# Kernel optimization log

Measured on AMD Instinct MI355X. Metric: run time of the kernel, lower is better.

The kernel has to match this reference:

```python
import jax, jax.numpy as jnp
import numpy as np

B, C, L, HEADS, DK = 32, 128, 32, 8, 64  # batch, channels, lattice side (L1=L2=L), heads, head dim
NLAYER = 4


def setup_inputs() -> dict:
    key = jax.random.key(0)
    ks = jax.random.split(key, 6)
    s_in = 1.0 / float(np.sqrt(C))          # lecun-normal scale for QKV (fan_in = channels)
    s_out = 1.0 / float(np.sqrt(HEADS * DK))  # lecun-normal scale for W0 (fan_in = dk*heads)
    return {
        "x": jax.random.normal(ks[0], (B, C, L, L), jnp.float32),
        "Wq": jax.random.normal(ks[1], (HEADS * DK, C), jnp.float32) * s_in,
        "Wk": jax.random.normal(ks[2], (HEADS * DK, C), jnp.float32) * s_in,
        "Wv": jax.random.normal(ks[3], (HEADS * DK, C), jnp.float32) * s_in,
        "R": jax.random.normal(ks[4], (HEADS, L, L), jnp.float32) * 0.02,
        "W0": jax.random.normal(ks[5], (C, HEADS * DK), jnp.float32) * s_out,
    }


def get_irpe(R):
    # r[h, i, j] = R[h, (xi - xj) mod L1, (yi - yj) mod L2]  (jnp negative indexing wraps)
    heads, L1, L2 = R.shape
    a1 = jnp.arange(L1)
    a2 = jnp.arange(L2)
    dx = (a1[:, None] - a1[None, :]) % L1        # (L1, L1)
    dy = (a2[:, None] - a2[None, :]) % L2        # (L2, L2)
    bias = R[:, dx[:, None, :, None], dy[None, :, None, :]]  # (heads, L1, L2, L1, L2)
    return bias.reshape(heads, L1 * L2, L1 * L2)


def reference(x, Wq, Wk, Wv, R, W0):
    bias = get_irpe(R)                            # (heads, N, N)
    inv_layer = 1.0 / float(np.sqrt(NLAYER + 1))
    inv_sqrt_dk = 1.0 / float(np.sqrt(DK))

    def block(xs):  # xs: (C, L, L) — single sample, as in the original __call__
        xn = xs * inv_layer
        xf = xn.reshape(C, -1)                    # (C, N)
        Q = (Wq @ xf).reshape(HEADS, DK, -1)      # 1x1 conv == matmul
        K = (Wk @ xf).reshape(HEADS, DK, -1)
        V = (Wv @ xf).reshape(HEADS, DK, -1)
        dot = jnp.einsum('hdi,hdj->hij', Q, K) + bias
        alpha = jax.nn.softmax(dot * inv_sqrt_dk, axis=-1)
        att = jnp.einsum('hij,hdj->hdi', alpha, V).reshape(HEADS * DK, -1)
        return (W0 @ att).reshape(xs.shape) + xs  # residual

    return jax.vmap(block)(x)
```

## Files before the change

kernel.cpp:

```cpp
#include <hip/hip_runtime.h>


#define NB   32
#define NH   8
#define SEQ  1024
#define DKH  64
#define HDIM 512
#define CIN  128

#define SCL 0.18033688011112042f

typedef __bf16 bf16x8 __attribute__((ext_vector_type(8)));
typedef float floatx4 __attribute__((ext_vector_type(4)));
typedef unsigned short u16x8 __attribute__((ext_vector_type(8)));
typedef unsigned int uintx4 __attribute__((ext_vector_type(4)));

__device__ __forceinline__ unsigned short f2bf(float f) {
    union { float f; unsigned int u; } c; c.f = f;
    unsigned int u = c.u;
    return (unsigned short)((u + 0x7fffu + ((u >> 16) & 1u)) >> 16);
}
__device__ __forceinline__ bf16x8 ldfrag(const unsigned short* p) {
    u16x8 v = *reinterpret_cast<const u16x8*>(p);
    return __builtin_bit_cast(bf16x8, v);
}
__device__ __forceinline__ unsigned int pkbf(float a, float b) {
    unsigned int ua = __builtin_bit_cast(unsigned int, a);
    unsigned int ub = __builtin_bit_cast(unsigned int, b);
    ua += 0x7fffu + ((ua >> 16) & 1u);
    ub += 0x7fffu + ((ub >> 16) & 1u);
    return __builtin_amdgcn_perm(ub, ua, 0x07060302u);
}
__device__ __forceinline__ unsigned int pkbf_t(float a, float b) {
    return __builtin_amdgcn_perm(__builtin_bit_cast(unsigned int, b),
                                 __builtin_bit_cast(unsigned int, a), 0x07060302u);
}
__device__ __forceinline__ void g2l16(const void* g, void* l) {
    __builtin_amdgcn_global_load_lds((const __attribute__((address_space(1))) void*)g,
                                     (__attribute__((address_space(3))) void*)l, 16, 0, 0);
}


__global__ __launch_bounds__(256) void prep_all(const float* __restrict__ Wq,
                                                const float* __restrict__ Wk,
                                                const float* __restrict__ Wv,
                                                const float* __restrict__ W0,
                                                const float* __restrict__ R,
                                                const float* __restrict__ x,
                                                unsigned short* __restrict__ w2,
                                                unsigned short* __restrict__ w0f,
                                                float* __restrict__ biasG,
                                                unsigned short* __restrict__ xt2) {
    __shared__ float lds[64 * 65];
    int bid = blockIdx.x;
    if (bid < 256) {
        int gidx = bid * 256 + threadIdx.x;
        int lane = gidx & 63, slot = gidx >> 6;
        int bb = slot & 1, a = (slot >> 1) & 1, dxx = (slot >> 2) & 31, h = slot >> 7;
        int q = lane >> 4, n = lane & 15;
        int iy = (a << 4) + n;
        const float* Rh = R + (h << 10) + (dxx << 5);
        floatx4 v;
        for (int r = 0; r < 4; ++r) {
            int jy = (bb << 4) + 4 * q + r;
            v[r] = Rh[(iy - jy) & 31] * SCL;
        }
        *(floatx4*)&biasG[(size_t)gidx * 4] = v;
    } else if (bid < 1280) {
        int idx = (bid - 256) * 256 + threadIdx.x;
        if (idx < 196608) {
            int row = idx >> 7, col = idx & 127;
            float v;
            if (row < 512)       v = Wq[idx] * SCL;
            else if (row < 1024) v = Wk[idx - 65536];
            else                 v = Wv[idx - 131072];
            int rt = row >> 4, nr = row & 15, kc = col >> 5, qc = (col & 31) >> 3, jc = col & 7;
            w2[((rt * 4 + kc) * 512) + (qc * 16 + nr) * 8 + jc] = f2bf(v);
        } else {
            int idx2 = idx - 196608;
            int row = idx2 >> 9, col = idx2 & 511;
            int rt = row >> 4, nr = row & 15, kcA = col >> 5, qc = (col & 31) >> 3, jc = col & 7;
            w0f[((rt * 16 + kcA) * 512) + (qc * 16 + nr) * 8 + jc] = f2bf(W0[idx2]);
        }
    } else {
        int r = bid - 1280;
        int b = r & 31, yy = (r >> 5) & 1, zz = r >> 6;
        int c0 = yy * 64, p0 = zz * 64;
        int t = threadIdx.x, tr = t >> 6, tc = t & 63;
        const float inv_layer = 0.44721359549995793f;
        for (int rr = 0; rr < 16; ++rr) {
            int cl = rr * 4 + tr;
            lds[cl * 65 + tc] = x[(b * CIN + c0 + cl) * SEQ + p0 + tc];
        }
        __syncthreads();
        for (int rr = 0; rr < 16; ++rr) {
            int pl = rr * 4 + tr;
            int pos = p0 + pl, c = c0 + tc;
            int pt = pos >> 4, np = pos & 15, kc = c >> 5, qc = (c & 31) >> 3, jc = c & 7;
            xt2[((size_t)((b * 64 + pt) * 4 + kc) * 512) + (qc * 16 + np) * 8 + jc] =
                f2bf(lds[tc * 65 + pl] * inv_layer);
        }
    }
}

__global__ __launch_bounds__(256, 4) void qkv_gemm(const unsigned short* __restrict__ xt2,
                                                   const unsigned short* __restrict__ w2,
                                                   unsigned short* __restrict__ Qt,
                                                   unsigned short* __restrict__ Kf,
                                                   unsigned short* __restrict__ Vf) {
    int b = blockIdx.x, y = blockIdx.y, zt = blockIdx.z;
    int tid = threadIdx.x, wave = tid >> 6, lane = tid & 63, q = lane >> 4, n = lane & 15;
    floatx4 acc[4];
    for (int s = 0; s < 4; ++s) acc[s] = (floatx4){0.f, 0.f, 0.f, 0.f};
    bf16x8 af[4], bfr[4][4];
    if (y < 16) {
        int rt = y * 4 + wave;
        const unsigned short* wbase = w2 + (size_t)rt * 4 * 512 + lane * 8;
        const unsigned short* xbase = xt2 + (size_t)(b * 64 + zt * 4) * 4 * 512 + lane * 8;
        for (int kc = 0; kc < 4; ++kc) af[kc] = ldfrag(wbase + kc * 512);
        for (int s = 0; s < 4; ++s)
            for (int kc = 0; kc < 4; ++kc) bfr[s][kc] = ldfrag(xbase + (s * 4 + kc) * 512);
        for (int kc = 0; kc < 4; ++kc)
            for (int s = 0; s < 4; ++s)
                acc[s] = __builtin_amdgcn_mfma_f32_16x16x32_bf16(af[kc], bfr[s][kc], acc[s], 0, 0, 0);
        int wrow0 = y * 64 + wave * 16;
        int pos0 = zt * 64;
        if (y < 8) {
            int h = wrow0 >> 6;
            int d0 = (wrow0 & 63) + 4 * q;
            for (int s = 0; s < 4; ++s) {
                uint2 pk;
                pk.x = pkbf(acc[s][0], acc[s][1]);
                pk.y = pkbf(acc[s][2], acc[s][3]);
                int pos = pos0 + 16 * s + n;
                *(uint2*)&Qt[((size_t)(b * NH + h) * SEQ + pos) * DKH + d0] = pk;
            }
        } else {
            int h = (wrow0 >> 6) - 8;
            int bh = b * NH + h;
            int cd = wave >> 1;
            int qk = 2 * (wave & 1) + (q >> 1);
            int jk = 4 * (q & 1);
            for (int s = 0; s < 4; ++s) {
                uint2 pk;
                pk.x = pkbf(acc[s][0], acc[s][1]);
                pk.y = pkbf(acc[s][2], acc[s][3]);
                size_t addr = ((size_t)(bh * 16 + zt) * 8 + s * 2 + cd) * 512
                              + (qk * 16 + n) * 8 + jk;
                *(uint2*)&Kf[addr] = pk;
            }
        }
    } else {
        int pt = zt * 4 + wave;
        const unsigned short* xbase = xt2 + (size_t)((b * 64 + pt) * 4) * 512 + lane * 8;
        int rtv0 = 64 + (y - 16) * 4;
        const unsigned short* wbase = w2 + (size_t)rtv0 * 4 * 512 + lane * 8;
        for (int kc = 0; kc < 4; ++kc) af[kc] = ldfrag(xbase + kc * 512);
        for (int s = 0; s < 4; ++s)
            for (int kc = 0; kc < 4; ++kc) bfr[s][kc] = ldfrag(wbase + (s * 4 + kc) * 512);
        for (int kc = 0; kc < 4; ++kc)
            for (int s = 0; s < 4; ++s)
                acc[s] = __builtin_amdgcn_mfma_f32_16x16x32_bf16(af[kc], bfr[s][kc], acc[s], 0, 0, 0);
        int vrow0 = (y - 16) * 64;
        int cj = wave >> 1;
        int jj0 = 4 * (wave & 1);
        for (int s = 0; s < 4; ++s) {
            int vrow = vrow0 + 16 * s + n;
            int h = vrow >> 6, d = vrow & 63;
            int u = d >> 4, nl = d & 15;
            uint2 pk;
            pk.x = pkbf(acc[s][0], acc[s][1]);
            pk.y = pkbf(acc[s][2], acc[s][3]);
            size_t addr = ((size_t)((b * NH + h) * 16 + zt) * 8 + u * 2 + cj) * 512
                          + (q * 16 + nl) * 8 + jj0;
            *(uint2*)&Vf[addr] = pk;
        }
    }
}

__global__ __launch_bounds__(256, 2) void attn_kernel(const unsigned short* __restrict__ Qt,
                                                      const unsigned short* __restrict__ Kf,
                                                      const unsigned short* __restrict__ Vf,
                                                      const float* __restrict__ biasG,
                                                      unsigned short* __restrict__ att2) {
    __shared__ alignas(16) unsigned short lds_k[2][8 * 512];
    __shared__ alignas(16) unsigned short lds_v[2][8 * 512];
    __shared__ alignas(16) float lds_bias[12 * 1024];

    int gid = blockIdx.x;
    int bh = gid & 255, qb = gid >> 8;
    int b = bh >> 3, h = bh & 7;
    int tid = threadIdx.x, wave = tid >> 6, lane = tid & 63, q = lane >> 4, n = lane & 15;
    int i0 = qb * 256 + wave * 64;
    int ti0 = i0 >> 4;

    const unsigned short* qbase = Qt + (size_t)bh * SEQ * DKH;
    const unsigned short* kft = Kf + (size_t)bh * 16 * 4096;
    const unsigned short* vft = Vf + (size_t)bh * 16 * 4096;
    const float* bGh = biasG + (size_t)h * 32768;

    bf16x8 aq[4][2];
    for (int qt = 0; qt < 4; ++qt)
        for (int c = 0; c < 2; ++c)
            aq[qt][c] = ldfrag(qbase + (i0 + 16 * qt + n) * DKH + c * 32 + q * 8);

    u16x8 ones_u;
    for (int t = 0; t < 8; ++t) ones_u[t] = 0x3F80;
    bf16x8 vone = __builtin_bit_cast(bf16x8, ones_u);

    floatx4 o[4][4], acc_l[4];
    for (int qt = 0; qt < 4; ++qt) {
        acc_l[qt] = (floatx4){0.f, 0.f, 0.f, 0.f};
        for (int u = 0; u < 4; ++u) o[qt][u] = (floatx4){0.f, 0.f, 0.f, 0.f};
    }

    int wb64 = qb * 8 + 255;
    int sbase = (qb * 8 + 47) % 12;
    int abb = (wave >> 1) * 2 + (wave & 1);
    int off0 = wave * 512;

    {
        for (int rel = 0; rel < 9; ++rel) {
            int dxx = (wb64 + rel) & 31;
            int phys = sbase + rel; if (phys >= 12) phys -= 12;
            g2l16(bGh + (dxx * 4 + abb) * 256 + lane * 4,
                  &lds_bias[(phys * 4 + abb) * 256]);
        }
        g2l16(kft + off0 + lane * 8,        &lds_k[0][off0]);
        g2l16(kft + 2048 + off0 + lane * 8, &lds_k[0][2048 + off0]);
        g2l16(vft + off0 + lane * 8,        &lds_v[0][off0]);
        g2l16(vft + 2048 + off0 + lane * 8, &lds_v[0][2048 + off0]);
    }
    __syncthreads();

#define LDB(qt, s0, s1, s2, s3) do {                                          \
        const float* bhi_ = ((qt) & 2) ? pb2 : pb1;                           \
        const float* blo_ = ((qt) & 2) ? pb1 : pb0;                           \
        const int ao_ = ((qt) & 1) << 9;                                      \
        s0 = *(const floatx4*)(bhi_ + ao_);                                   \
        s1 = *(const floatx4*)(bhi_ + ao_ + 256);                             \
        s2 = *(const floatx4*)(blo_ + ao_);                                   \
        s3 = *(const floatx4*)(blo_ + ao_ + 256);                             \
    } while (0)

#define SMM(qt, s0, s1, s2, s3) do {                                          \
        s0 = __builtin_amdgcn_mfma_f32_16x16x32_bf16(kf2[0][0], aq[qt][0], s0, 0, 0, 0); \
        s0 = __builtin_amdgcn_mfma_f32_16x16x32_bf16(kf2[0][1], aq[qt][1], s0, 0, 0, 0); \
        s1 = __builtin_amdgcn_mfma_f32_16x16x32_bf16(kf2[1][0], aq[qt][0], s1, 0, 0, 0); \
        s1 = __builtin_amdgcn_mfma_f32_16x16x32_bf16(kf2[1][1], aq[qt][1], s1, 0, 0, 0); \
        s2 = __builtin_amdgcn_mfma_f32_16x16x32_bf16(kf2[2][0], aq[qt][0], s2, 0, 0, 0); \
        s2 = __builtin_amdgcn_mfma_f32_16x16x32_bf16(kf2[2][1], aq[qt][1], s2, 0, 0, 0); \
        s3 = __builtin_amdgcn_mfma_f32_16x16x32_bf16(kf2[3][0], aq[qt][0], s3, 0, 0, 0); \
        s3 = __builtin_amdgcn_mfma_f32_16x16x32_bf16(kf2[3][1], aq[qt][1], s3, 0, 0, 0); \
    } while (0)

#define EPO(qt, s0, s1, s2, s3) do {                                          \
        uintx4 pu0_, pu1_;                                                    \
        pu0_[0] = pkbf_t(__builtin_amdgcn_exp2f(s0[0]), __builtin_amdgcn_exp2f(s0[1])); \
        pu0_[1] = pkbf_t(__builtin_amdgcn_exp2f(s0[2]), __builtin_amdgcn_exp2f(s0[3])); \
        pu0_[2] = pkbf_t(__builtin_amdgcn_exp2f(s1[0]), __builtin_amdgcn_exp2f(s1[1])); \
        pu0_[3] = pkbf_t(__builtin_amdgcn_exp2f(s1[2]), __builtin_amdgcn_exp2f(s1[3])); \
        pu1_[0] = pkbf_t(__builtin_amdgcn_exp2f(s2[0]), __builtin_amdgcn_exp2f(s2[1])); \
        pu1_[1] = pkbf_t(__builtin_amdgcn_exp2f(s2[2]), __builtin_amdgcn_exp2f(s2[3])); \
        pu1_[2] = pkbf_t(__builtin_amdgcn_exp2f(s3[0]), __builtin_amdgcn_exp2f(s3[1])); \
        pu1_[3] = pkbf_t(__builtin_amdgcn_exp2f(s3[2]), __builtin_amdgcn_exp2f(s3[3])); \
        bf16x8 pf0_ = __builtin_bit_cast(bf16x8, pu0_);                       \
        bf16x8 pf1_ = __builtin_bit_cast(bf16x8, pu1_);                       \
        acc_l[qt] = __builtin_amdgcn_mfma_f32_16x16x32_bf16(vone, pf0_, acc_l[qt], 0, 0, 0); \
        acc_l[qt] = __builtin_amdgcn_mfma_f32_16x16x32_bf16(vone, pf1_, acc_l[qt], 0, 0, 0); \
        o[qt][0] = __builtin_amdgcn_mfma_f32_16x16x32_bf16(vf2[0][0], pf0_, o[qt][0], 0, 0, 0); \
        o[qt][0] = __builtin_amdgcn_mfma_f32_16x16x32_bf16(vf2[0][1], pf1_, o[qt][0], 0, 0, 0); \
        o[qt][1] = __builtin_amdgcn_mfma_f32_16x16x32_bf16(vf2[1][0], pf0_, o[qt][1], 0, 0, 0); \
        o[qt][1] = __builtin_amdgcn_mfma_f32_16x16x32_bf16(vf2[1][1], pf1_, o[qt][1], 0, 0, 0); \
        o[qt][2] = __builtin_amdgcn_mfma_f32_16x16x32_bf16(vf2[2][0], pf0_, o[qt][2], 0, 0, 0); \
        o[qt][2] = __builtin_amdgcn_mfma_f32_16x16x32_bf16(vf2[2][1], pf1_, o[qt][2], 0, 0, 0); \
        o[qt][3] = __builtin_amdgcn_mfma_f32_16x16x32_bf16(vf2[3][0], pf0_, o[qt][3], 0, 0, 0); \
        o[qt][3] = __builtin_amdgcn_mfma_f32_16x16x32_bf16(vf2[3][1], pf1_, o[qt][3], 0, 0, 0); \
    } while (0)

    for (int kt = 0; kt < 16; ++kt) {
        int cur = kt & 1;
        int t0 = sbase - 2; if (t0 < 0) t0 += 12;

        if (kt < 15) {
            const unsigned short* kg = kft + (kt + 1) * 4096;
            const unsigned short* vg = vft + (kt + 1) * 4096;
            unsigned short* dk = &lds_k[cur ^ 1][0];
            unsigned short* dv = &lds_v[cur ^ 1][0];
            g2l16(kg + off0 + lane * 8,        dk + off0);
            g2l16(kg + 2048 + off0 + lane * 8, dk + 2048 + off0);
            g2l16(vg + off0 + lane * 8,        dv + off0);
            g2l16(vg + 2048 + off0 + lane * 8, dv + 2048 + off0);
            int t1 = t0 + 1; if (t1 >= 12) t1 -= 12;
            int dx0 = (wb64 - 2) & 31;
            int dx1 = (wb64 - 1) & 31;
            g2l16(bGh + (dx0 * 4 + abb) * 256 + lane * 4,
                  &lds_bias[(t0 * 4 + abb) * 256]);
            g2l16(bGh + (dx1 * 4 + abb) * 256 + lane * 4,
                  &lds_bias[(t1 * 4 + abb) * 256]);
        }

        int r0 = sbase + 2 * wave; if (r0 >= 12) r0 -= 12;
        int r1 = r0 + 1; if (r1 >= 12) r1 -= 12;
        int r2 = r0 + 2; if (r2 >= 12) r2 -= 12;
        const float* pb0 = &lds_bias[r0 * 1024 + lane * 4];
        const float* pb1 = &lds_bias[r1 * 1024 + lane * 4];
        const float* pb2 = &lds_bias[r2 * 1024 + lane * 4];

        bf16x8 kf2[4][2], vf2[4][2];
#pragma unroll
        for (int s = 0; s < 4; ++s)
#pragma unroll
            for (int c = 0; c < 2; ++c) {
                kf2[s][c] = ldfrag(&lds_k[cur][(s * 2 + c) * 512 + lane * 8]);
                vf2[s][c] = ldfrag(&lds_v[cur][(s * 2 + c) * 512 + lane * 8]);
            }

        floatx4 sA0, sA1, sA2, sA3, sB0, sB1, sB2, sB3;
        LDB(0, sA0, sA1, sA2, sA3);
        SMM(0, sA0, sA1, sA2, sA3);
        LDB(1, sB0, sB1, sB2, sB3);
        SMM(1, sB0, sB1, sB2, sB3);
        EPO(0, sA0, sA1, sA2, sA3);
        LDB(2, sA0, sA1, sA2, sA3);
        SMM(2, sA0, sA1, sA2, sA3);
        EPO(1, sB0, sB1, sB2, sB3);
        LDB(3, sB0, sB1, sB2, sB3);
        SMM(3, sB0, sB1, sB2, sB3);
        EPO(2, sA0, sA1, sA2, sA3);
        EPO(3, sB0, sB1, sB2, sB3);

        sbase = t0;
        wb64 -= 2;
        __syncthreads();
    }

#undef LDB
#undef SMM
#undef EPO

    for (int qt = 0; qt < 4; ++qt) {
        float inv = 1.0f / acc_l[qt][0];
        int pt = ti0 + qt;
        for (int u = 0; u < 4; ++u) {
            int kcA = 2 * h + (u >> 1);
            int q2 = 2 * (u & 1) + (q >> 1);
            uint2 pk;
            pk.x = pkbf(o[qt][u][0] * inv, o[qt][u][1] * inv);
            pk.y = pkbf(o[qt][u][2] * inv, o[qt][u][3] * inv);
            size_t addr = ((size_t)((b * 64 + pt) * 16 + kcA) * 512)
                          + (q2 * 16 + n) * 8 + 4 * (q & 1);
            *(uint2*)&att2[addr] = pk;
        }
    }
}

__global__ __launch_bounds__(256, 4) void out_gemm(const unsigned short* __restrict__ att2,
                                                   const unsigned short* __restrict__ w0f,
                                                   const float* __restrict__ x,
                                                   float* __restrict__ out) {
    int b = blockIdx.x, ct = blockIdx.y, ptb = blockIdx.z;
    int tid = threadIdx.x, wave = tid >> 6, lane = tid & 63, q = lane >> 4, n = lane & 15;
    int pos0 = ptb * 64 + wave * 16;
    int c0 = ct * 64;
    int pt = ptb * 4 + wave;
    const unsigned short* abase = att2 + (size_t)(b * 64 + pt) * 16 * 512 + lane * 8;
    const unsigned short* wbase = w0f + (size_t)(c0 >> 4) * 16 * 512 + lane * 8;
    floatx4 acc[4];
    for (int s = 0; s < 4; ++s) acc[s] = (floatx4){0.f, 0.f, 0.f, 0.f};
    for (int g = 0; g < 4; ++g) {
        bf16x8 af[4], bfr[4][4];
        for (int k2 = 0; k2 < 4; ++k2) af[k2] = ldfrag(abase + (g * 4 + k2) * 512);
        for (int s = 0; s < 4; ++s)
            for (int k2 = 0; k2 < 4; ++k2)
                bfr[s][k2] = ldfrag(wbase + (s * 16 + g * 4 + k2) * 512);
        for (int k2 = 0; k2 < 4; ++k2)
            for (int s = 0; s < 4; ++s)
                acc[s] = __builtin_amdgcn_mfma_f32_16x16x32_bf16(af[k2], bfr[s][k2], acc[s], 0, 0, 0);
    }
    int p0q = pos0 + 4 * q;
    for (int s = 0; s < 4; ++s) {
        int c = c0 + 16 * s + n;
        size_t idx = ((size_t)b * CIN + c) * SEQ + p0q;
        floatx4 res = *(const floatx4*)&x[idx];
        floatx4 v = acc[s] + res;
        *(floatx4*)&out[idx] = v;
    }
}

extern "C" void kernel_launch(void* const* d_in, const int* in_sizes, int n_in,
                              void* d_out, int out_size, void* d_ws, size_t ws_size,
                              hipStream_t stream) {
    const float* x  = (const float*)d_in[0];
    const float* Wq = (const float*)d_in[1];
    const float* Wk = (const float*)d_in[2];
    const float* Wv = (const float*)d_in[3];
    const float* R  = (const float*)d_in[4];
    const float* W0 = (const float*)d_in[5];
    float* out = (float*)d_out;

    char* ws = (char*)d_ws;
    size_t off = 0;
    unsigned short* Qt   = (unsigned short*)(ws + off); off += (size_t)NB * NH * SEQ * DKH * 2;
    unsigned short* Kf   = (unsigned short*)(ws + off); off += (size_t)NB * NH * SEQ * DKH * 2;
    unsigned short* Vf   = (unsigned short*)(ws + off); off += (size_t)NB * NH * SEQ * DKH * 2;
    unsigned short* att2 = (unsigned short*)(ws + off); off += (size_t)NB * SEQ * HDIM * 2;
    unsigned short* xt2  = (unsigned short*)(ws + off); off += (size_t)NB * SEQ * CIN * 2;
    unsigned short* w2   = (unsigned short*)(ws + off); off += (size_t)1536 * 128 * 2;
    unsigned short* w0f  = (unsigned short*)(ws + off); off += (size_t)128 * 512 * 2;
    float* biasG = (float*)(ws + off); off += (size_t)NH * 32 * 4 * 256 * 4;
    (void)ws_size; (void)in_sizes; (void)n_in; (void)out_size;

    prep_all<<<2304, 256, 0, stream>>>(Wq, Wk, Wv, W0, R, x, w2, w0f, biasG, xt2);
    qkv_gemm<<<dim3(NB, 24, 16), 256, 0, stream>>>(xt2, w2, Qt, Kf, Vf);
    attn_kernel<<<NB * NH * 4, 256, 0, stream>>>(Qt, Kf, Vf, biasG, att2);
    out_gemm<<<dim3(NB, 2, 16), 256, 0, stream>>>(att2, w0f, x, out);
}
```

Before: 212.4 us.

## Store compact per-head circulant bias in LDS instead of streaming expanded bias tiles

Replaces the expanded bias tensor (per head, per dx, fragment-shaped tiles streamed through a 12-slot LDS ring buffer) with a compact 32x36 table per head built from R. Attention blocks load it once into LDS and index it with lane-dependent offsets, which removes the per-iteration bias global loads and shrinks LDS from about 48KB to about 4.5KB per block. Launch bounds rise to 3 blocks per CU to use the freed LDS. The trade-offs are scalar, possibly bank-conflicting LDS reads in place of vector reads, tighter register limits at occupancy 3, and a bias prep that now runs on a single block.

```diff
diff --git a/kernel.cpp b/kernel.cpp
--- a/kernel.cpp
+++ b/kernel.cpp
@@ -49,25 +49,21 @@
                                                 const float* __restrict__ x,
                                                 unsigned short* __restrict__ w2,
                                                 unsigned short* __restrict__ w0f,
-                                                float* __restrict__ biasG,
+                                                float* __restrict__ biasR,
                                                 unsigned short* __restrict__ xt2) {
     __shared__ float lds[64 * 65];
     int bid = blockIdx.x;
-    if (bid < 256) {
-        int gidx = bid * 256 + threadIdx.x;
-        int lane = gidx & 63, slot = gidx >> 6;
-        int bb = slot & 1, a = (slot >> 1) & 1, dxx = (slot >> 2) & 31, h = slot >> 7;
-        int q = lane >> 4, n = lane & 15;
-        int iy = (a << 4) + n;
-        const float* Rh = R + (h << 10) + (dxx << 5);
-        floatx4 v;
-        for (int r = 0; r < 4; ++r) {
-            int jy = (bb << 4) + 4 * q + r;
-            v[r] = Rh[(iy - jy) & 31] * SCL;
-        }
-        *(floatx4*)&biasG[(size_t)gidx * 4] = v;
-    } else if (bid < 1280) {
-        int idx = (bid - 256) * 256 + threadIdx.x;
+    if (bid == 0) {
+        for (int i = 0; i < 36; ++i) {
+            int e = threadIdx.x * 36 + i;
+            int h = e / 1152;
+            int rem = e - h * 1152;
+            int dxx = rem / 36;
+            int t = rem - dxx * 36;
+            biasR[e] = R[(h << 10) + (dxx << 5) + ((32 - t) & 31)] * SCL;
+        }
+    } else if (bid < 1025) {
+        int idx = (bid - 1) * 256 + threadIdx.x;
         if (idx < 196608) {
             int row = idx >> 7, col = idx & 127;
             float v;
@@ -83,7 +79,7 @@
             w0f[((rt * 16 + kcA) * 512) + (qc * 16 + nr) * 8 + jc] = f2bf(W0[idx2]);
         }
     } else {
-        int r = bid - 1280;
+        int r = bid - 1025;
         int b = r & 31, yy = (r >> 5) & 1, zz = r >> 6;
         int c0 = yy * 64, p0 = zz * 64;
         int t = threadIdx.x, tr = t >> 6, tc = t & 63;
@@ -178,14 +174,14 @@
     }
 }
 
-__global__ __launch_bounds__(256, 2) void attn_kernel(const unsigned short* __restrict__ Qt,
+__global__ __launch_bounds__(256, 3) void attn_kernel(const unsigned short* __restrict__ Qt,
                                                       const unsigned short* __restrict__ Kf,
                                                       const unsigned short* __restrict__ Vf,
-                                                      const float* __restrict__ biasG,
+                                                      const float* __restrict__ biasR,
                                                       unsigned short* __restrict__ att2) {
     __shared__ alignas(16) unsigned short lds_k[2][8 * 512];
     __shared__ alignas(16) unsigned short lds_v[2][8 * 512];
-    __shared__ alignas(16) float lds_bias[12 * 1024];
+    __shared__ alignas(16) float lds_bR[32 * 36];
 
     int gid = blockIdx.x;
     int bh = gid & 255, qb = gid >> 8;
@@ -197,7 +193,19 @@
     const unsigned short* qbase = Qt + (size_t)bh * SEQ * DKH;
     const unsigned short* kft = Kf + (size_t)bh * 16 * 4096;
     const unsigned short* vft = Vf + (size_t)bh * 16 * 4096;
-    const float* bGh = biasG + (size_t)h * 32768;
+
+    {
+        const float* bRg = biasR + h * 1152;
+        for (int i = tid; i < 288; i += 256) {
+            floatx4 v = *(const floatx4*)&bRg[i * 4];
+            *(floatx4*)&lds_bR[i * 4] = v;
+        }
+        int off0 = wave * 512;
+        g2l16(kft + off0 + lane * 8,        &lds_k[0][off0]);
+        g2l16(kft + 2048 + off0 + lane * 8, &lds_k[0][2048 + off0]);
+        g2l16(vft + off0 + lane * 8,        &lds_v[0][off0]);
+        g2l16(vft + 2048 + off0 + lane * 8, &lds_v[0][2048 + off0]);
+    }
 
     bf16x8 aq[4][2];
     for (int qt = 0; qt < 4; ++qt)
@@ -214,33 +222,23 @@
         for (int u = 0; u < 4; ++u) o[qt][u] = (floatx4){0.f, 0.f, 0.f, 0.f};
     }
 
-    int wb64 = qb * 8 + 255;
-    int sbase = (qb * 8 + 47) % 12;
-    int abb = (wave >> 1) * 2 + (wave & 1);
-    int off0 = wave * 512;
-
-    {
-        for (int rel = 0; rel < 9; ++rel) {
-            int dxx = (wb64 + rel) & 31;
-            int phys = sbase + rel; if (phys >= 12) phys -= 12;
-            g2l16(bGh + (dxx * 4 + abb) * 256 + lane * 4,
-                  &lds_bias[(phys * 4 + abb) * 256]);
-        }
-        g2l16(kft + off0 + lane * 8,        &lds_k[0][off0]);
-        g2l16(kft + 2048 + off0 + lane * 8, &lds_k[0][2048 + off0]);
-        g2l16(vft + off0 + lane * 8,        &lds_v[0][off0]);
-        g2l16(vft + 2048 + off0 + lane * 8, &lds_v[0][2048 + off0]);
-    }
+    int st0 = (4 * q - n) & 31;
+    int st1 = (st0 + 16) & 31;
+    const float* pst0 = lds_bR + st0;
+    const float* pst1 = lds_bR + st1;
+    int ee = qb * 8 + 2 * wave;
+
     __syncthreads();
 
 #define LDB(qt, s0, s1, s2, s3) do {                                          \
-        const float* bhi_ = ((qt) & 2) ? pb2 : pb1;                           \
-        const float* blo_ = ((qt) & 2) ? pb1 : pb0;                           \
-        const int ao_ = ((qt) & 1) << 9;                                      \
-        s0 = *(const floatx4*)(bhi_ + ao_);                                   \
-        s1 = *(const floatx4*)(bhi_ + ao_ + 256);                             \
-        s2 = *(const floatx4*)(blo_ + ao_);                                   \
-        s3 = *(const floatx4*)(blo_ + ao_ + 256);                             \
+        int dh_ = ((ee + ((qt) >> 1)) & 31) * 36;                             \
+        int dl_ = ((ee + ((qt) >> 1) - 1) & 31) * 36;                         \
+        const float* pA_ = ((qt) & 1) ? pst1 : pst0;                          \
+        const float* pB_ = ((qt) & 1) ? pst0 : pst1;                          \
+        s0 = (floatx4){pA_[dh_], pA_[dh_ + 1], pA_[dh_ + 2], pA_[dh_ + 3]};   \
+        s1 = (floatx4){pB_[dh_], pB_[dh_ + 1], pB_[dh_ + 2], pB_[dh_ + 3]};   \
+        s2 = (floatx4){pA_[dl_], pA_[dl_ + 1], pA_[dl_ + 2], pA_[dl_ + 3]};   \
+        s3 = (floatx4){pB_[dl_], pB_[dl_ + 1], pB_[dl_ + 2], pB_[dl_ + 3]};   \
     } while (0)
 
 #define SMM(qt, s0, s1, s2, s3) do {                                          \
@@ -280,32 +278,18 @@
 
     for (int kt = 0; kt < 16; ++kt) {
         int cur = kt & 1;
-        int t0 = sbase - 2; if (t0 < 0) t0 += 12;
 
         if (kt < 15) {
             const unsigned short* kg = kft + (kt + 1) * 4096;
             const unsigned short* vg = vft + (kt + 1) * 4096;
             unsigned short* dk = &lds_k[cur ^ 1][0];
             unsigned short* dv = &lds_v[cur ^ 1][0];
+            int off0 = wave * 512;
             g2l16(kg + off0 + lane * 8,        dk + off0);
             g2l16(kg + 2048 + off0 + lane * 8, dk + 2048 + off0);
             g2l16(vg + off0 + lane * 8,        dv + off0);
             g2l16(vg + 2048 + off0 + lane * 8, dv + 2048 + off0);
-            int t1 = t0 + 1; if (t1 >= 12) t1 -= 12;
-            int dx0 = (wb64 - 2) & 31;
-            int dx1 = (wb64 - 1) & 31;
-            g2l16(bGh + (dx0 * 4 + abb) * 256 + lane * 4,
-                  &lds_bias[(t0 * 4 + abb) * 256]);
-            g2l16(bGh + (dx1 * 4 + abb) * 256 + lane * 4,
-                  &lds_bias[(t1 * 4 + abb) * 256]);
-        }
-
-        int r0 = sbase + 2 * wave; if (r0 >= 12) r0 -= 12;
-        int r1 = r0 + 1; if (r1 >= 12) r1 -= 12;
-        int r2 = r0 + 2; if (r2 >= 12) r2 -= 12;
-        const float* pb0 = &lds_bias[r0 * 1024 + lane * 4];
-        const float* pb1 = &lds_bias[r1 * 1024 + lane * 4];
-        const float* pb2 = &lds_bias[r2 * 1024 + lane * 4];
+        }
 
         bf16x8 kf2[4][2], vf2[4][2];
 #pragma unroll
@@ -330,8 +314,7 @@
         EPO(2, sA0, sA1, sA2, sA3);
         EPO(3, sB0, sB1, sB2, sB3);
 
-        sbase = t0;
-        wb64 -= 2;
+        ee -= 2;
         __syncthreads();
     }
 
@@ -408,11 +391,11 @@
     unsigned short* xt2  = (unsigned short*)(ws + off); off += (size_t)NB * SEQ * CIN * 2;
     unsigned short* w2   = (unsigned short*)(ws + off); off += (size_t)1536 * 128 * 2;
     unsigned short* w0f  = (unsigned short*)(ws + off); off += (size_t)128 * 512 * 2;
-    float* biasG = (float*)(ws + off); off += (size_t)NH * 32 * 4 * 256 * 4;
+    float* biasR = (float*)(ws + off); off += (size_t)NH * 32 * 36 * 4;
     (void)ws_size; (void)in_sizes; (void)n_in; (void)out_size;
 
-    prep_all<<<2304, 256, 0, stream>>>(Wq, Wk, Wv, W0, R, x, w2, w0f, biasG, xt2);
+    prep_all<<<2049, 256, 0, stream>>>(Wq, Wk, Wv, W0, R, x, w2, w0f, biasR, xt2);
     qkv_gemm<<<dim3(NB, 24, 16), 256, 0, stream>>>(xt2, w2, Qt, Kf, Vf);
-    attn_kernel<<<NB * NH * 4, 256, 0, stream>>>(Qt, Kf, Vf, biasG, att2);
+    attn_kernel<<<NB * NH * 4, 256, 0, stream>>>(Qt, Kf, Vf, biasR, att2);
     out_gemm<<<dim3(NB, 2, 16), 256, 0, stream>>>(att2, w0f, x, out);
 }
```

Result: slower. 418.0 us (+96.8%).
